# Optimization experiments

Hardware: AMD Instinct MI355X
Metric: run time of the kernel (lower is better)

Reference implementation:

```python
import jax, jax.numpy as jnp
import numpy as np
import math

IN_FEATURES = 1024
OUT_FEATURES = 1024
N_BANK = 8192
N_LAYER = 12
N_EMBD = 1024


def setup_inputs() -> dict:
    key = jax.random.key(0)
    kq, kk, kv = jax.random.split(key, 3)
    q = jax.random.normal(kq, (4, 2048, IN_FEATURES), dtype=jnp.float32)
    k = 0.02 * jax.random.normal(kk, (N_BANK, IN_FEATURES), dtype=jnp.float32)
    v_std = 2.0 / N_LAYER / math.sqrt(N_EMBD)
    v = v_std * jax.random.normal(kv, (N_BANK, OUT_FEATURES), dtype=jnp.float32)
    return {"q": q, "k": k, "v": v}


def reference(q, k, v):
    # scores: [B, T, N]
    scores = jnp.einsum("btd,nd->btn", q, k)
    # row-wise L2 normalization, scaled by sqrt(N), then exact (erf) GELU
    sqrt_n = jnp.sqrt(jnp.asarray(scores.shape[-1], scores.dtype))
    norm = jnp.linalg.norm(scores, axis=-1, keepdims=True)
    gated = jax.nn.gelu(scores / norm * sqrt_n, approximate=False)
    # out: [B, T, out_features]
    return jnp.einsum("btn,no->bto", gated, v)
```

## Files before the change

### kernel.cpp

```cpp
#include <hip/hip_runtime.h>
#include <hip/hip_bf16.h>
#include <math.h>


#define MROWS 8192
#define DIN   1024
#define NBANK 8192
#define DOUT  1024

typedef float  f32x4  __attribute__((ext_vector_type(4)));
typedef __bf16 bf16x8 __attribute__((ext_vector_type(8)));

__device__ __forceinline__ float bf2f(unsigned short u) {
  union { unsigned int i; float f; } x; x.i = ((unsigned int)u) << 16; return x.f;
}
__device__ __forceinline__ unsigned short f2bf(float f) {
  union { float f; unsigned int i; } x; x.f = f;
  unsigned int u = x.i;
  unsigned int r = (u + 0x7fffu + ((u >> 16) & 1u)) >> 16;
  return (unsigned short)r;
}

__global__ void cvt_kernel(const float* __restrict__ src,
                           unsigned short* __restrict__ dst, int n) {
  int i = (blockIdx.x * 256 + threadIdx.x) * 4;
  if (i >= n) return;
  float4 vv = *(const float4*)(src + i);
  ushort4 o;
  o.x = f2bf(vv.x); o.y = f2bf(vv.y); o.z = f2bf(vv.z); o.w = f2bf(vv.w);
  *(ushort4*)(dst + i) = o;
}

__global__ void transpose_cvt_kernel(const float* __restrict__ src,
                                     unsigned short* __restrict__ dst,
                                     int R, int C) {
  __shared__ float tile[32][33];
  int c0 = blockIdx.x * 32, r0 = blockIdx.y * 32;
  for (int i = threadIdx.y; i < 32; i += 8)
    tile[i][threadIdx.x] = src[(size_t)(r0 + i) * C + c0 + threadIdx.x];
  __syncthreads();
  for (int i = threadIdx.y; i < 32; i += 8)
    dst[(size_t)(c0 + i) * R + r0 + threadIdx.x] = f2bf(tile[threadIdx.x][i]);
}

__global__ void zero_f32_kernel(float* __restrict__ p, int n4) {
  int i = blockIdx.x * 256 + threadIdx.x;
  if (i < n4) ((float4*)p)[i] = make_float4(0.f, 0.f, 0.f, 0.f);
}

__global__ __launch_bounds__(256, 2) void gemm1_kernel(
    const unsigned short* __restrict__ A, const unsigned short* __restrict__ B,
    unsigned short* __restrict__ C, float* __restrict__ sumsq) {
  __shared__ unsigned short As[128 * 32];
  __shared__ unsigned short Bs[128 * 32];
  const int K = DIN, ldc = NBANK;

  const int tid  = threadIdx.x;
  const int lane = tid & 63;
  const int wave = tid >> 6;
  const int wm   = (wave >> 1) * 64;
  const int wn   = (wave & 1) * 64;
  const int quad = lane >> 4;
  const int l16  = lane & 15;

  const int flat = blockIdx.y * gridDim.x + blockIdx.x;
  const int nwg  = gridDim.x * gridDim.y;
  const int swz  = (flat & 7) * (nwg >> 3) + (flat >> 3);
  const size_t m0 = (size_t)(swz / gridDim.x) * 128;
  const size_t n0 = (size_t)(swz % gridDim.x) * 128;

  const int srow = tid >> 2;
  const int scol = (tid & 3) * 8;
  const unsigned short* Ag0 = A + (m0 + srow) * (size_t)K + scol;
  const unsigned short* Ag1 = A + (m0 + srow + 64) * (size_t)K + scol;
  const unsigned short* Bg0 = B + (n0 + srow) * (size_t)K + scol;
  const unsigned short* Bg1 = B + (n0 + srow + 64) * (size_t)K + scol;

  unsigned short* AsW0 = As + tid * 8;
  unsigned short* AsW1 = As + 64 * 32 + tid * 8;
  unsigned short* BsW0 = Bs + tid * 8;
  unsigned short* BsW1 = Bs + 64 * 32 + tid * 8;

  const unsigned short* ArP = As + (wm + l16) * 32 + quad * 8;
  const unsigned short* BrP = Bs + (wn + l16) * 32 + quad * 8;

  f32x4 acc[4][4];
#pragma unroll
  for (int i = 0; i < 4; i++)
#pragma unroll
    for (int j = 0; j < 4; j++) {
      f32x4 z = {0.f, 0.f, 0.f, 0.f};
      acc[i][j] = z;
    }

  for (int k0 = 0; k0 < K; k0 += 32) {
    __builtin_amdgcn_global_load_lds(
        (const __attribute__((address_space(1))) unsigned int*)(Ag0 + k0),
        (__attribute__((address_space(3))) unsigned int*)AsW0, 16, 0, 0);
    __builtin_amdgcn_global_load_lds(
        (const __attribute__((address_space(1))) unsigned int*)(Ag1 + k0),
        (__attribute__((address_space(3))) unsigned int*)AsW1, 16, 0, 0);
    __builtin_amdgcn_global_load_lds(
        (const __attribute__((address_space(1))) unsigned int*)(Bg0 + k0),
        (__attribute__((address_space(3))) unsigned int*)BsW0, 16, 0, 0);
    __builtin_amdgcn_global_load_lds(
        (const __attribute__((address_space(1))) unsigned int*)(Bg1 + k0),
        (__attribute__((address_space(3))) unsigned int*)BsW1, 16, 0, 0);
    __syncthreads();

    bf16x8 af[4], bfr[4];
#pragma unroll
    for (int i = 0; i < 4; i++) af[i] = *(const bf16x8*)(ArP + i * 16 * 32);
#pragma unroll
    for (int j = 0; j < 4; j++) bfr[j] = *(const bf16x8*)(BrP + j * 16 * 32);
#pragma unroll
    for (int i = 0; i < 4; i++)
#pragma unroll
      for (int j = 0; j < 4; j++)
        acc[i][j] = __builtin_amdgcn_mfma_f32_16x16x32_bf16(af[i], bfr[j],
                                                            acc[i][j], 0, 0, 0);
    __syncthreads();
  }

#pragma unroll
  for (int i = 0; i < 4; i++)
#pragma unroll
    for (int r = 0; r < 4; r++) {
      size_t row = m0 + wm + i * 16 + quad * 4 + r;
      float s = 0.f;
#pragma unroll
      for (int j = 0; j < 4; j++) {
        float val = acc[i][j][r];
        s += val * val;
        C[row * (size_t)ldc + n0 + wn + j * 16 + l16] = f2bf(val);
      }
      s += __shfl_xor(s, 1);
      s += __shfl_xor(s, 2);
      s += __shfl_xor(s, 4);
      s += __shfl_xor(s, 8);
      if (l16 == 0) atomicAdd(&sumsq[row], s);
    }
}

__global__ void gelu_kernel(unsigned short* __restrict__ S,
                            const float* __restrict__ sumsq) {
  const size_t total = (size_t)MROWS * NBANK / 8;
  for (size_t u = (size_t)blockIdx.x * 256 + threadIdx.x; u < total;
       u += (size_t)gridDim.x * 256) {
    size_t idx = u * 8;
    int row = (int)(idx >> 13);
    float sc = sqrtf((float)NBANK / sumsq[row]);
    uint4 vv = *(const uint4*)(S + idx);
    unsigned int w[4] = {vv.x, vv.y, vv.z, vv.w};
#pragma unroll
    for (int e = 0; e < 4; e++) {
      float x0 = bf2f((unsigned short)(w[e] & 0xffffu)) * sc;
      float x1 = bf2f((unsigned short)(w[e] >> 16)) * sc;
      float g0 = 0.5f * x0 * (1.0f + erff(x0 * 0.70710678118654752f));
      float g1 = 0.5f * x1 * (1.0f + erff(x1 * 0.70710678118654752f));
      w[e] = (unsigned int)f2bf(g0) | ((unsigned int)f2bf(g1) << 16);
    }
    uint4 o; o.x = w[0]; o.y = w[1]; o.z = w[2]; o.w = w[3];
    *(uint4*)(S + idx) = o;
  }
}

__global__ __launch_bounds__(512, 4) void gemm2_kernel(
    const unsigned short* __restrict__ A,
    const unsigned short* __restrict__ B,
    float* __restrict__ C) {
  __shared__ unsigned short As[128 * 32];
  __shared__ unsigned short Bs[256 * 32];
  const int K = NBANK, ldc = DOUT;

  const int tid  = threadIdx.x;
  const int lane = tid & 63;
  const int wave = tid >> 6;
  const int wm   = (wave >> 2) * 64;
  const int wn   = (wave & 3) * 64;
  const int quad = lane >> 4;
  const int l16  = lane & 15;

  const int flat = blockIdx.y * gridDim.x + blockIdx.x;
  const int nwg  = gridDim.x * gridDim.y;
  const int swz  = (flat & 7) * (nwg >> 3) + (flat >> 3);
  const size_t m0 = (size_t)(swz / gridDim.x) * 128;
  const size_t n0 = (size_t)(swz % gridDim.x) * 256;
  const int    ks = blockIdx.z * (K / 2);

  const int srow = tid >> 2;
  const int scol = (tid & 3) * 8;
  const unsigned short* Ag  = A + (m0 + srow) * (size_t)K + scol + ks;
  const unsigned short* Bg0 = B + (n0 + srow) * (size_t)K + scol + ks;
  const unsigned short* Bg1 = B + (n0 + srow + 128) * (size_t)K + scol + ks;

  unsigned short* AsW  = As + tid * 8;
  unsigned short* BsW0 = Bs + tid * 8;
  unsigned short* BsW1 = Bs + 512 * 8 + tid * 8;

  const unsigned short* ArP = As + (wm + l16) * 32 + quad * 8;
  const unsigned short* BrP = Bs + (wn + l16) * 32 + quad * 8;

  f32x4 acc[4][4];
#pragma unroll
  for (int i = 0; i < 4; i++)
#pragma unroll
    for (int j = 0; j < 4; j++) {
      f32x4 z = {0.f, 0.f, 0.f, 0.f};
      acc[i][j] = z;
    }

  for (int k0 = 0; k0 < K / 2; k0 += 32) {
    __builtin_amdgcn_global_load_lds(
        (const __attribute__((address_space(1))) unsigned int*)(Ag + k0),
        (__attribute__((address_space(3))) unsigned int*)AsW, 16, 0, 0);
    __builtin_amdgcn_global_load_lds(
        (const __attribute__((address_space(1))) unsigned int*)(Bg0 + k0),
        (__attribute__((address_space(3))) unsigned int*)BsW0, 16, 0, 0);
    __builtin_amdgcn_global_load_lds(
        (const __attribute__((address_space(1))) unsigned int*)(Bg1 + k0),
        (__attribute__((address_space(3))) unsigned int*)BsW1, 16, 0, 0);
    __syncthreads();

    bf16x8 af[4], bfr[4];
#pragma unroll
    for (int i = 0; i < 4; i++) af[i] = *(const bf16x8*)(ArP + i * 16 * 32);
#pragma unroll
    for (int j = 0; j < 4; j++) bfr[j] = *(const bf16x8*)(BrP + j * 16 * 32);
#pragma unroll
    for (int i = 0; i < 4; i++)
#pragma unroll
      for (int j = 0; j < 4; j++)
        acc[i][j] = __builtin_amdgcn_mfma_f32_16x16x32_bf16(af[i], bfr[j],
                                                            acc[i][j], 0, 0, 0);
    __syncthreads();
  }

#pragma unroll
  for (int i = 0; i < 4; i++)
#pragma unroll
    for (int j = 0; j < 4; j++)
#pragma unroll
      for (int r = 0; r < 4; r++) {
        size_t row = m0 + wm + i * 16 + quad * 4 + r;
        size_t col = n0 + wn + j * 16 + l16;
        atomicAdd(&C[row * (size_t)ldc + col], acc[i][j][r]);
      }
}

extern "C" void kernel_launch(void* const* d_in, const int* in_sizes, int n_in,
                              void* d_out, int out_size, void* d_ws, size_t ws_size,
                              hipStream_t stream) {
  const float* q = (const float*)d_in[0];
  const float* k = (const float*)d_in[1];
  const float* v = (const float*)d_in[2];
  float* out = (float*)d_out;

  char* ws = (char*)d_ws;
  const size_t MB = 1024ull * 1024ull;
  unsigned short* qb     = (unsigned short*)(ws);
  unsigned short* kb     = (unsigned short*)(ws + 16 * MB);
  unsigned short* vbT    = (unsigned short*)(ws + 32 * MB);
  unsigned short* scores = (unsigned short*)(ws + 48 * MB);
  float*          scale  = (float*)(ws + 176 * MB);

  const int nqk = MROWS * DIN;

  zero_f32_kernel<<<(MROWS * DOUT / 4 + 255) / 256, 256, 0, stream>>>(out,
                                                                      MROWS * DOUT / 4);
  zero_f32_kernel<<<(MROWS / 4 + 255) / 256, 256, 0, stream>>>(scale, MROWS / 4);

  cvt_kernel<<<nqk / 1024, 256, 0, stream>>>(q, qb, nqk);
  cvt_kernel<<<nqk / 1024, 256, 0, stream>>>(k, kb, nqk);
  transpose_cvt_kernel<<<dim3(DOUT / 32, NBANK / 32), dim3(32, 8), 0, stream>>>(
      v, vbT, NBANK, DOUT);

  gemm1_kernel<<<dim3(NBANK / 128, MROWS / 128), 256, 0, stream>>>(qb, kb, scores,
                                                                   scale);

  gelu_kernel<<<4096, 256, 0, stream>>>(scores, scale);

  gemm2_kernel<<<dim3(DOUT / 256, MROWS / 128, 2), 512, 0, stream>>>(scores, vbT, out);
}
```

Measured before the change: 614.0 us.

## Fuse prep kernels, swizzle LDS, drop split-K atomics in gemm2

Merges the q/k conversion, v transpose-convert, and sumsq zeroing into one prep kernel, and drops zeroing of the output. Both GEMMs get an XOR swizzle on the global-to-LDS column offset and the matching fragment reads, aimed at avoiding LDS bank conflicts. gemm2 drops split-K and atomics, using 128x128 tiles over the full K with plain stores. This gives fewer launches and no atomic traffic, but gemm2 now runs 512 blocks with long K loops, which may underfill the device.

```diff
diff --git a/kernel.cpp b/kernel.cpp
--- a/kernel.cpp
+++ b/kernel.cpp
@@ -21,31 +21,36 @@
   return (unsigned short)r;
 }
 
-__global__ void cvt_kernel(const float* __restrict__ src,
-                           unsigned short* __restrict__ dst, int n) {
-  int i = (blockIdx.x * 256 + threadIdx.x) * 4;
-  if (i >= n) return;
-  float4 vv = *(const float4*)(src + i);
-  ushort4 o;
-  o.x = f2bf(vv.x); o.y = f2bf(vv.y); o.z = f2bf(vv.z); o.w = f2bf(vv.w);
-  *(ushort4*)(dst + i) = o;
-}
-
-__global__ void transpose_cvt_kernel(const float* __restrict__ src,
-                                     unsigned short* __restrict__ dst,
-                                     int R, int C) {
+__global__ void prep_kernel(const float* __restrict__ q, const float* __restrict__ k,
+                            const float* __restrict__ v,
+                            unsigned short* __restrict__ qb,
+                            unsigned short* __restrict__ kb,
+                            unsigned short* __restrict__ vbT,
+                            float* __restrict__ sumsq) {
   __shared__ float tile[32][33];
-  int c0 = blockIdx.x * 32, r0 = blockIdx.y * 32;
-  for (int i = threadIdx.y; i < 32; i += 8)
-    tile[i][threadIdx.x] = src[(size_t)(r0 + i) * C + c0 + threadIdx.x];
-  __syncthreads();
-  for (int i = threadIdx.y; i < 32; i += 8)
-    dst[(size_t)(c0 + i) * R + r0 + threadIdx.x] = f2bf(tile[threadIdx.x][i]);
-}
-
-__global__ void zero_f32_kernel(float* __restrict__ p, int n4) {
-  int i = blockIdx.x * 256 + threadIdx.x;
-  if (i < n4) ((float4*)p)[i] = make_float4(0.f, 0.f, 0.f, 0.f);
+  const int b = blockIdx.x;
+  if (b < 16384) {
+    const float* src = (b < 8192) ? q : k;
+    unsigned short* dst = (b < 8192) ? qb : kb;
+    int i = ((b & 8191) * 256 + threadIdx.x) * 4;
+    float4 vv = *(const float4*)(src + i);
+    ushort4 o;
+    o.x = f2bf(vv.x); o.y = f2bf(vv.y); o.z = f2bf(vv.z); o.w = f2bf(vv.w);
+    *(ushort4*)(dst + i) = o;
+  } else if (b < 24576) {
+    int t = b - 16384;
+    int c0 = (t & 31) * 32;
+    int r0 = (t >> 5) * 32;
+    int tx = threadIdx.x & 31, ty = threadIdx.x >> 5;
+    for (int i = ty; i < 32; i += 8)
+      tile[i][tx] = v[(size_t)(r0 + i) * DOUT + c0 + tx];
+    __syncthreads();
+    for (int i = ty; i < 32; i += 8)
+      vbT[(size_t)(c0 + i) * NBANK + r0 + tx] = f2bf(tile[tx][i]);
+  } else {
+    int i = (b - 24576) * 256 + threadIdx.x;
+    ((float4*)sumsq)[i] = make_float4(0.f, 0.f, 0.f, 0.f);
+  }
 }
 
 __global__ __launch_bounds__(256, 2) void gemm1_kernel(
@@ -53,7 +58,7 @@
     unsigned short* __restrict__ C, float* __restrict__ sumsq) {
   __shared__ unsigned short As[128 * 32];
   __shared__ unsigned short Bs[128 * 32];
-  const int K = DIN, ldc = NBANK;
+  const int K = DIN;
 
   const int tid  = threadIdx.x;
   const int lane = tid & 63;
@@ -70,7 +75,7 @@
   const size_t n0 = (size_t)(swz % gridDim.x) * 128;
 
   const int srow = tid >> 2;
-  const int scol = (tid & 3) * 8;
+  const int scol = (((tid & 3) ^ ((tid >> 3) & 3))) * 8;
   const unsigned short* Ag0 = A + (m0 + srow) * (size_t)K + scol;
   const unsigned short* Ag1 = A + (m0 + srow + 64) * (size_t)K + scol;
   const unsigned short* Bg0 = B + (n0 + srow) * (size_t)K + scol;
@@ -81,8 +86,9 @@
   unsigned short* BsW0 = Bs + tid * 8;
   unsigned short* BsW1 = Bs + 64 * 32 + tid * 8;
 
-  const unsigned short* ArP = As + (wm + l16) * 32 + quad * 8;
-  const unsigned short* BrP = Bs + (wn + l16) * 32 + quad * 8;
+  const int sw = (l16 >> 1) & 3;
+  const unsigned short* ArP = As + (wm + l16) * 32 + (quad ^ sw) * 8;
+  const unsigned short* BrP = Bs + (wn + l16) * 32 + (quad ^ sw) * 8;
 
   f32x4 acc[4][4];
 #pragma unroll
@@ -132,7 +138,7 @@
       for (int j = 0; j < 4; j++) {
         float val = acc[i][j][r];
         s += val * val;
-        C[row * (size_t)ldc + n0 + wn + j * 16 + l16] = f2bf(val);
+        C[row * (size_t)NBANK + n0 + wn + j * 16 + l16] = f2bf(val);
       }
       s += __shfl_xor(s, 1);
       s += __shfl_xor(s, 2);
@@ -165,19 +171,19 @@
   }
 }
 
-__global__ __launch_bounds__(512, 4) void gemm2_kernel(
+__global__ __launch_bounds__(256, 4) void gemm2_kernel(
     const unsigned short* __restrict__ A,
     const unsigned short* __restrict__ B,
     float* __restrict__ C) {
   __shared__ unsigned short As[128 * 32];
-  __shared__ unsigned short Bs[256 * 32];
+  __shared__ unsigned short Bs[128 * 32];
   const int K = NBANK, ldc = DOUT;
 
   const int tid  = threadIdx.x;
   const int lane = tid & 63;
   const int wave = tid >> 6;
-  const int wm   = (wave >> 2) * 64;
-  const int wn   = (wave & 3) * 64;
+  const int wm   = (wave >> 1) * 64;
+  const int wn   = (wave & 1) * 64;
   const int quad = lane >> 4;
   const int l16  = lane & 15;
 
@@ -185,21 +191,23 @@
   const int nwg  = gridDim.x * gridDim.y;
   const int swz  = (flat & 7) * (nwg >> 3) + (flat >> 3);
   const size_t m0 = (size_t)(swz / gridDim.x) * 128;
-  const size_t n0 = (size_t)(swz % gridDim.x) * 256;
-  const int    ks = blockIdx.z * (K / 2);
+  const size_t n0 = (size_t)(swz % gridDim.x) * 128;
 
   const int srow = tid >> 2;
-  const int scol = (tid & 3) * 8;
-  const unsigned short* Ag  = A + (m0 + srow) * (size_t)K + scol + ks;
-  const unsigned short* Bg0 = B + (n0 + srow) * (size_t)K + scol + ks;
-  const unsigned short* Bg1 = B + (n0 + srow + 128) * (size_t)K + scol + ks;
-
-  unsigned short* AsW  = As + tid * 8;
+  const int scol = (((tid & 3) ^ ((tid >> 3) & 3))) * 8;
+  const unsigned short* Ag0 = A + (m0 + srow) * (size_t)K + scol;
+  const unsigned short* Ag1 = A + (m0 + srow + 64) * (size_t)K + scol;
+  const unsigned short* Bg0 = B + (n0 + srow) * (size_t)K + scol;
+  const unsigned short* Bg1 = B + (n0 + srow + 64) * (size_t)K + scol;
+
+  unsigned short* AsW0 = As + tid * 8;
+  unsigned short* AsW1 = As + 64 * 32 + tid * 8;
   unsigned short* BsW0 = Bs + tid * 8;
-  unsigned short* BsW1 = Bs + 512 * 8 + tid * 8;
-
-  const unsigned short* ArP = As + (wm + l16) * 32 + quad * 8;
-  const unsigned short* BrP = Bs + (wn + l16) * 32 + quad * 8;
+  unsigned short* BsW1 = Bs + 64 * 32 + tid * 8;
+
+  const int sw = (l16 >> 1) & 3;
+  const unsigned short* ArP = As + (wm + l16) * 32 + (quad ^ sw) * 8;
+  const unsigned short* BrP = Bs + (wn + l16) * 32 + (quad ^ sw) * 8;
 
   f32x4 acc[4][4];
 #pragma unroll
@@ -210,10 +218,13 @@
       acc[i][j] = z;
     }
 
-  for (int k0 = 0; k0 < K / 2; k0 += 32) {
-    __builtin_amdgcn_global_load_lds(
-        (const __attribute__((address_space(1))) unsigned int*)(Ag + k0),
-        (__attribute__((address_space(3))) unsigned int*)AsW, 16, 0, 0);
+  for (int k0 = 0; k0 < K; k0 += 32) {
+    __builtin_amdgcn_global_load_lds(
+        (const __attribute__((address_space(1))) unsigned int*)(Ag0 + k0),
+        (__attribute__((address_space(3))) unsigned int*)AsW0, 16, 0, 0);
+    __builtin_amdgcn_global_load_lds(
+        (const __attribute__((address_space(1))) unsigned int*)(Ag1 + k0),
+        (__attribute__((address_space(3))) unsigned int*)AsW1, 16, 0, 0);
     __builtin_amdgcn_global_load_lds(
         (const __attribute__((address_space(1))) unsigned int*)(Bg0 + k0),
         (__attribute__((address_space(3))) unsigned int*)BsW0, 16, 0, 0);
@@ -244,7 +255,7 @@
       for (int r = 0; r < 4; r++) {
         size_t row = m0 + wm + i * 16 + quad * 4 + r;
         size_t col = n0 + wn + j * 16 + l16;
-        atomicAdd(&C[row * (size_t)ldc + col], acc[i][j][r]);
+        C[row * (size_t)ldc + col] = acc[i][j][r];
       }
 }
 
@@ -264,21 +275,12 @@
   unsigned short* scores = (unsigned short*)(ws + 48 * MB);
   float*          scale  = (float*)(ws + 176 * MB);
 
-  const int nqk = MROWS * DIN;
-
-  zero_f32_kernel<<<(MROWS * DOUT / 4 + 255) / 256, 256, 0, stream>>>(out,
-                                                                      MROWS * DOUT / 4);
-  zero_f32_kernel<<<(MROWS / 4 + 255) / 256, 256, 0, stream>>>(scale, MROWS / 4);
-
-  cvt_kernel<<<nqk / 1024, 256, 0, stream>>>(q, qb, nqk);
-  cvt_kernel<<<nqk / 1024, 256, 0, stream>>>(k, kb, nqk);
-  transpose_cvt_kernel<<<dim3(DOUT / 32, NBANK / 32), dim3(32, 8), 0, stream>>>(
-      v, vbT, NBANK, DOUT);
+  prep_kernel<<<24584, 256, 0, stream>>>(q, k, v, qb, kb, vbT, scale);
 
   gemm1_kernel<<<dim3(NBANK / 128, MROWS / 128), 256, 0, stream>>>(qb, kb, scores,
                                                                    scale);
 
   gelu_kernel<<<4096, 256, 0, stream>>>(scores, scale);
 
-  gemm2_kernel<<<dim3(DOUT / 256, MROWS / 128, 2), 512, 0, stream>>>(scores, vbT, out);
-}
+  gemm2_kernel<<<dim3(DOUT / 128, MROWS / 128), 256, 0, stream>>>(scores, vbT, out);
+}
```

Result: faster. 561.0 us (-8.6%).
